# Optimization experiments

Hardware: AMD Instinct MI355X
Metric: run time of the kernel (lower is better)

Reference implementation:

```python
import jax, jax.numpy as jnp
import numpy as np

N, E = 100000, 400000
IN_DIM, PAD_DIM, HID = 384, 3, 64

def _xavier(key, fan_in, fan_out, shape=None):
    shape = shape or (fan_in, fan_out)
    lim = float(np.sqrt(6.0 / (fan_in + fan_out)))
    return jax.random.uniform(key, shape, jnp.float32, -lim, lim)

def setup_inputs():
    key = jax.random.key(0)
    ks = jax.random.split(key, 20)
    return {
        "x": jax.random.normal(ks[0], (N, IN_DIM), jnp.float32),
        "edge_index": jax.random.randint(ks[1], (2, E), 0, N),
        "pad_state": jax.random.uniform(ks[2], (PAD_DIM,), jnp.float32, -1.0, 1.0),
        # GAT layer 1: in = IN_DIM+PAD_DIM, heads=4, out=HID per head
        "W1": _xavier(ks[3], IN_DIM + PAD_DIM, 4 * HID),
        "att_src1": _xavier(ks[4], HID, HID, (4, HID)),
        "att_dst1": _xavier(ks[5], HID, HID, (4, HID)),
        "b1": jnp.zeros((4 * HID,), jnp.float32),
        # GAT layer 2: in = 4*HID, heads=2
        "W2": _xavier(ks[6], 4 * HID, 2 * HID),
        "att_src2": _xavier(ks[7], HID, HID, (2, HID)),
        "att_dst2": _xavier(ks[8], HID, HID, (2, HID)),
        "b2": jnp.zeros((2 * HID,), jnp.float32),
        # attention-score MLP
        "aw1": _xavier(ks[9], 2 * HID, HID),
        "ab1": jnp.zeros((HID,), jnp.float32),
        "aw2": _xavier(ks[10], HID, 1),
        "ab2": jnp.zeros((1,), jnp.float32),
        # emotion gate
        "gw": _xavier(ks[11], PAD_DIM, HID),
        "gb": jnp.zeros((HID,), jnp.float32),
    }

def _gat(h_in, src, dst, W, a_src, a_dst, bias, heads):
    # PyG GATConv (eval mode): linear -> per-head LeakyReLU attention logits
    # -> edge softmax over destination -> scatter-add aggregation -> concat heads + bias
    n = h_in.shape[0]
    h = (h_in @ W).reshape(n, heads, -1)               # [N,H,C]
    al_s = jnp.einsum('nhc,hc->nh', h, a_src)          # [N,H]
    al_d = jnp.einsum('nhc,hc->nh', h, a_dst)
    e = jax.nn.leaky_relu(al_s[src] + al_d[dst], 0.2)  # [Etot,H]
    m = jax.ops.segment_max(e, dst, num_segments=n)    # stable softmax per dst
    p = jnp.exp(e - m[dst])
    denom = jax.ops.segment_sum(p, dst, num_segments=n)
    coef = p / (denom[dst] + 1e-16)
    out = jax.ops.segment_sum(h[src] * coef[:, :, None], dst, num_segments=n)
    return out.reshape(n, -1) + bias

def reference(x, edge_index, pad_state, W1, att_src1, att_dst1, b1,
              W2, att_src2, att_dst2, b2, aw1, ab1, aw2, ab2, gw, gb):
    n = x.shape[0]
    loops = jnp.arange(n, dtype=edge_index.dtype)      # add_self_loops=True default
    src = jnp.concatenate([edge_index[0], loops])
    dst = jnp.concatenate([edge_index[1], loops])
    pad_exp = jnp.broadcast_to(pad_state.reshape(1, -1), (n, pad_state.size))
    h = jnp.concatenate([x, pad_exp], axis=-1)         # [N, in_dim+pad_dim]
    h = jax.nn.elu(_gat(h, src, dst, W1, att_src1, att_dst1, b1, 4))
    h = jax.nn.elu(_gat(h, src, dst, W2, att_src2, att_dst2, b2, 2))
    gate = jax.nn.sigmoid(pad_exp @ gw + gb)           # [N,HID]
    h = h * jnp.tile(gate, (1, 2))                     # [N,2*HID]
    attn = jax.nn.sigmoid(jax.nn.relu(h @ aw1 + ab1) @ aw2 + ab2)  # [N,1]
    return h, attn
```

## Files before the change

kernel.cpp:

```cpp
#include <hip/hip_runtime.h>
#include <hip/hip_bf16.h>
#include <stdint.h>

#define IN_DIM 384
#define HID 64
#define C1 256
#define C2 128

typedef unsigned int uint32;
typedef __bf16 bf16x8 __attribute__((ext_vector_type(8)));
typedef float f32x4 __attribute__((ext_vector_type(4)));

static __device__ __forceinline__ float bf2f(unsigned short u){
    return __uint_as_float(((uint32)u) << 16);
}
static __device__ __forceinline__ unsigned short f2bf(float x){
    uint32 u = __float_as_uint(x);
    return (unsigned short)((u + 0x7FFFu + ((u >> 16) & 1u)) >> 16);
}
static __device__ __forceinline__ uint32 pack2(float a, float b){
    return (uint32)f2bf(a) | ((uint32)f2bf(b) << 16);
}

__global__ void k_zero(int* deg, int* cur, int N){
    int i = blockIdx.x*256 + threadIdx.x;
    if (i < N){ deg[i] = 0; cur[i] = 0; }
}
__global__ void k_hist(const int* __restrict__ ei, int* deg, int E){
    int i = blockIdx.x*256 + threadIdx.x;
    if (i < E) atomicAdd(&deg[ei[E + i]], 1);
}
__global__ void k_scan1(const int* __restrict__ deg, int* rowptr, int* part, int N){
    __shared__ int s[256];
    int tid = threadIdx.x;
    int i = blockIdx.x*256 + tid;
    int v = (i < N) ? deg[i] : 0;
    s[tid] = v; __syncthreads();
    for (int off = 1; off < 256; off <<= 1){
        int t = (tid >= off) ? s[tid - off] : 0;
        __syncthreads();
        s[tid] += t;
        __syncthreads();
    }
    if (i < N) rowptr[i] = s[tid] - v;
    if (tid == 255) part[blockIdx.x] = s[tid];
}
__global__ void k_scan2(int* part, int nb){
    __shared__ int s[512];
    int tid = threadIdx.x;
    int v = (tid < nb) ? part[tid] : 0;
    s[tid] = v; __syncthreads();
    for (int off = 1; off < 512; off <<= 1){
        int t = (tid >= off) ? s[tid - off] : 0;
        __syncthreads();
        s[tid] += t;
        __syncthreads();
    }
    if (tid < nb) part[tid] = s[tid] - v;
}
__global__ void k_scan3(int* rowptr, const int* __restrict__ part, int N, int E){
    int i = blockIdx.x*256 + threadIdx.x;
    if (i < N) rowptr[i] += part[blockIdx.x];
    if (i == 0) rowptr[N] = E;
}
__global__ void k_scatter(const int* __restrict__ ei, const int* __restrict__ rowptr,
                          int* cur, int* colx, int* dstx, int E){
    int i = blockIdx.x*256 + threadIdx.x;
    if (i < E){
        int d = ei[E + i];
        int pos = atomicAdd(&cur[d], 1);
        int p = rowptr[d] + pos;
        colx[p] = ei[i];
        dstx[p] = d;
    }
}

__global__ __launch_bounds__(256) void k_cvtW(const float* __restrict__ W,
        unsigned short* __restrict__ Wf, int ncol, int ntiles, int nunits){
    int unit = blockIdx.x*4 + (threadIdx.x >> 6);
    if (unit >= nunits) return;
    int l = threadIdx.x & 63;
    int s = unit / ntiles, ct = unit % ntiles;
    int col = ct*16 + (l & 15);
    int g = l >> 4;
    unsigned short o[8];
    #pragma unroll
    for (int j = 0; j < 8; j++){
        int k = s*32 + g*8 + j;
        o[j] = f2bf(W[(size_t)k*ncol + col]);
    }
    ushort4* dst = (ushort4*)&Wf[((size_t)unit*64 + l)*8];
    dst[0] = make_ushort4(o[0], o[1], o[2], o[3]);
    dst[1] = make_ushort4(o[4], o[5], o[6], o[7]);
}

__global__ __launch_bounds__(256) void k_prep(const float* __restrict__ W1,
        const float* __restrict__ pad, const float* __restrict__ gw, const float* __restrict__ gb,
        float* __restrict__ c1v, float* __restrict__ gate){
    int tid = threadIdx.x;
    c1v[tid] = pad[0]*W1[(size_t)(IN_DIM+0)*C1 + tid]
             + pad[1]*W1[(size_t)(IN_DIM+1)*C1 + tid]
             + pad[2]*W1[(size_t)(IN_DIM+2)*C1 + tid];
    if (tid < HID){
        float g = pad[0]*gw[0*HID + tid] + pad[1]*gw[1*HID + tid] + pad[2]*gw[2*HID + tid] + gb[tid];
        gate[tid] = 1.f/(1.f + __expf(-g));
    }
}

__global__ __launch_bounds__(256) void k_gemm1_mfma(const float* __restrict__ x,
        const unsigned short* __restrict__ Wf, const float* __restrict__ c1v,
        const float* __restrict__ as1, const float* __restrict__ ad1,
        unsigned short* __restrict__ h1, float* __restrict__ als, float* __restrict__ ald, int N)
{
    __shared__ unsigned short Af[12*4*64*8];
    const int tid = threadIdx.x;
    const int l   = tid & 63;
    const int w   = tid >> 6;
    const int n0  = blockIdx.x * 64;

    const int srow = w*16 + (l & 15);
    const int kc   = l >> 4;
    int crow = n0 + srow; if (crow > N-1) crow = N-1;
    const float* xr = x + (size_t)crow*IN_DIM + kc*8;

    float4 a0[12], a1[12];
    #pragma unroll
    for (int j = 0; j < 12; j++){
        a0[j] = *(const float4*)(xr + j*32);
        a1[j] = *(const float4*)(xr + j*32 + 4);
    }
    #pragma unroll
    for (int j = 0; j < 12; j++){
        uint4 u;
        u.x = pack2(a0[j].x, a0[j].y); u.y = pack2(a0[j].z, a0[j].w);
        u.z = pack2(a1[j].x, a1[j].y); u.w = pack2(a1[j].z, a1[j].w);
        *(uint4*)&Af[((j*4 + w)*64 + l)*8] = u;
    }

    f32x4 acc[4][4];
    #pragma unroll
    for (int i = 0; i < 4; i++)
        #pragma unroll
        for (int rt = 0; rt < 4; rt++)
            acc[i][rt] = (f32x4){0.f, 0.f, 0.f, 0.f};

    uint4 wcur[4], wnxt[4];
    {
        const unsigned short* p = Wf + ((size_t)(w*4)*64 + l)*8;
        #pragma unroll
        for (int i = 0; i < 4; i++) wcur[i] = *(const uint4*)(p + (size_t)i*512);
    }
    __syncthreads();

    for (int ku = 0; ku < 12; ++ku){
        if (ku < 11){
            const unsigned short* p = Wf + ((size_t)((ku+1)*16 + w*4)*64 + l)*8;
            #pragma unroll
            for (int i = 0; i < 4; i++) wnxt[i] = *(const uint4*)(p + (size_t)i*512);
        }
        bf16x8 af[4];
        #pragma unroll
        for (int rt = 0; rt < 4; rt++)
            af[rt] = __builtin_bit_cast(bf16x8, *(const uint4*)&Af[((ku*4 + rt)*64 + l)*8]);
        #pragma unroll
        for (int i = 0; i < 4; i++){
            bf16x8 bw = __builtin_bit_cast(bf16x8, wcur[i]);
            #pragma unroll
            for (int rt = 0; rt < 4; rt++)
                acc[i][rt] = __builtin_amdgcn_mfma_f32_16x16x32_bf16(bw, af[rt], acc[i][rt], 0, 0, 0);
        }
        if (ku < 11){
            #pragma unroll
            for (int i = 0; i < 4; i++) wcur[i] = wnxt[i];
        }
    }

    const int g = l >> 4;
    float4 cvv[4], av[4], dv[4];
    #pragma unroll
    for (int i = 0; i < 4; i++){
        int cl = i*16 + g*4;
        cvv[i] = *(const float4*)&c1v[w*64 + cl];
        av[i]  = *(const float4*)&as1[w*64 + cl];
        dv[i]  = *(const float4*)&ad1[w*64 + cl];
    }
    #pragma unroll
    for (int rt = 0; rt < 4; rt++){
        int node = n0 + rt*16 + (l & 15);
        bool ok = node < N;
        float ps = 0.f, pd = 0.f;
        #pragma unroll
        for (int i = 0; i < 4; i++){
            float h0 = acc[i][rt][0] + cvv[i].x;
            float h1v = acc[i][rt][1] + cvv[i].y;
            float h2v = acc[i][rt][2] + cvv[i].z;
            float h3v = acc[i][rt][3] + cvv[i].w;
            ps += h0*av[i].x + h1v*av[i].y + h2v*av[i].z + h3v*av[i].w;
            pd += h0*dv[i].x + h1v*dv[i].y + h2v*dv[i].z + h3v*dv[i].w;
            if (ok){
                ushort4 o = make_ushort4(f2bf(h0), f2bf(h1v), f2bf(h2v), f2bf(h3v));
                *(ushort4*)&h1[(size_t)node*C1 + w*64 + i*16 + g*4] = o;
            }
        }
        ps += __shfl_xor(ps, 16, 64); ps += __shfl_xor(ps, 32, 64);
        pd += __shfl_xor(pd, 16, 64); pd += __shfl_xor(pd, 32, 64);
        if (ok && g == 0){
            als[(size_t)node*4 + w] = ps;
            ald[(size_t)node*4 + w] = pd;
        }
    }
}

__global__ __launch_bounds__(256) void k_gemm2_mfma(const unsigned short* __restrict__ x2,
        const unsigned short* __restrict__ Wf,
        const float* __restrict__ as2, const float* __restrict__ ad2,
        unsigned short* __restrict__ h2, float* __restrict__ als, float* __restrict__ ald, int N)
{
    __shared__ unsigned short Af[2][4*64*8];
    const int tid = threadIdx.x;
    const int l   = tid & 63;
    const int w   = tid >> 6;
    const int wr  = w >> 1, wc = w & 1;
    const int n0  = blockIdx.x * 64;

    const int sr  = tid >> 2;
    const int kc  = tid & 3;
    const int d0  = ((sr >> 4)*64 + kc*16 + (sr & 15))*8;
    int crow = n0 + sr; if (crow > N-1) crow = N-1;
    const unsigned short* xrow = x2 + (size_t)crow*C1 + kc*8;

    f32x4 acc[4][2];
    #pragma unroll
    for (int i = 0; i < 4; i++)
        #pragma unroll
        for (int rt = 0; rt < 2; rt++)
            acc[i][rt] = (f32x4){0.f, 0.f, 0.f, 0.f};

    uint4 p0, wcur[4], wnxt[4];
    p0 = *(const uint4*)(xrow);
    *(uint4*)&Af[0][d0] = p0;
    {
        const unsigned short* p = Wf + ((size_t)(wc*4)*64 + l)*8;
        #pragma unroll
        for (int i = 0; i < 4; i++) wcur[i] = *(const uint4*)(p + (size_t)i*512);
    }
    __syncthreads();

    for (int s = 0; s < 8; ++s){
        if (s < 7){
            p0 = *(const uint4*)(xrow + (s+1)*32);
            const unsigned short* p = Wf + ((size_t)((s+1)*8 + wc*4)*64 + l)*8;
            #pragma unroll
            for (int i = 0; i < 4; i++) wnxt[i] = *(const uint4*)(p + (size_t)i*512);
        }
        bf16x8 af[2];
        #pragma unroll
        for (int rt = 0; rt < 2; rt++)
            af[rt] = __builtin_bit_cast(bf16x8, *(const uint4*)&Af[s&1][((wr*2 + rt)*64 + l)*8]);
        #pragma unroll
        for (int i = 0; i < 4; i++){
            bf16x8 bw = __builtin_bit_cast(bf16x8, wcur[i]);
            #pragma unroll
            for (int rt = 0; rt < 2; rt++)
                acc[i][rt] = __builtin_amdgcn_mfma_f32_16x16x32_bf16(bw, af[rt], acc[i][rt], 0, 0, 0);
        }
        if (s < 7){
            *(uint4*)&Af[(s+1)&1][d0] = p0;
            __syncthreads();
            #pragma unroll
            for (int i = 0; i < 4; i++) wcur[i] = wnxt[i];
        }
    }

    const int g = l >> 4;
    float4 av[4], dv[4];
    #pragma unroll
    for (int i = 0; i < 4; i++){
        int cl = i*16 + g*4;
        av[i] = *(const float4*)&as2[wc*64 + cl];
        dv[i] = *(const float4*)&ad2[wc*64 + cl];
    }
    #pragma unroll
    for (int rt = 0; rt < 2; rt++){
        int node = n0 + wr*32 + rt*16 + (l & 15);
        bool ok = node < N;
        float ps = 0.f, pd = 0.f;
        #pragma unroll
        for (int i = 0; i < 4; i++){
            float h0 = acc[i][rt][0], h1v = acc[i][rt][1];
            float h2v = acc[i][rt][2], h3v = acc[i][rt][3];
            ps += h0*av[i].x + h1v*av[i].y + h2v*av[i].z + h3v*av[i].w;
            pd += h0*dv[i].x + h1v*dv[i].y + h2v*dv[i].z + h3v*dv[i].w;
            if (ok){
                ushort4 o = make_ushort4(f2bf(h0), f2bf(h1v), f2bf(h2v), f2bf(h3v));
                *(ushort4*)&h2[(size_t)node*C2 + wc*64 + i*16 + g*4] = o;
            }
        }
        ps += __shfl_xor(ps, 16, 64); ps += __shfl_xor(ps, 32, 64);
        pd += __shfl_xor(pd, 16, 64); pd += __shfl_xor(pd, 32, 64);
        if (ok && g == 0){
            als[(size_t)node*2 + wc] = ps;
            ald[(size_t)node*2 + wc] = pd;
        }
    }
}

template<int H>
__global__ __launch_bounds__(256) void k_elogit(const int* __restrict__ colx,
        const int* __restrict__ dstx, const float* __restrict__ als,
        const float* __restrict__ ald, float* __restrict__ ep, int E)
{
    int i = blockIdx.x*256 + threadIdx.x;
    if (i >= E) return;
    int s = colx[i], d = dstx[i];
    if constexpr (H == 4){
        float4 a = *(const float4*)&als[(size_t)s*4];
        float4 b = *(const float4*)&ald[(size_t)d*4];
        float4 e;
        e.x = a.x + b.x; e.x = fmaxf(e.x, 0.2f*e.x);
        e.y = a.y + b.y; e.y = fmaxf(e.y, 0.2f*e.y);
        e.z = a.z + b.z; e.z = fmaxf(e.z, 0.2f*e.z);
        e.w = a.w + b.w; e.w = fmaxf(e.w, 0.2f*e.w);
        *(float4*)&ep[(size_t)i*4] = e;
    } else {
        float2 a = *(const float2*)&als[(size_t)s*2];
        float2 b = *(const float2*)&ald[(size_t)d*2];
        float2 e;
        e.x = a.x + b.x; e.x = fmaxf(e.x, 0.2f*e.x);
        e.y = a.y + b.y; e.y = fmaxf(e.y, 0.2f*e.y);
        *(float2*)&ep[(size_t)i*2] = e;
    }
}

template<int H>
__global__ __launch_bounds__(256) void k_segsm(const int* __restrict__ rowptr,
        const float* __restrict__ als, const float* __restrict__ ald,
        float* __restrict__ ep, float* __restrict__ den, float* __restrict__ pSelf, int NH)
{
    int t = blockIdx.x*256 + threadIdx.x;
    if (t >= NH) return;
    int node = t / H;
    int head = t - node*H;
    int base = rowptr[node];
    int cnt  = rowptr[node+1] - base;
    float es = als[t] + ald[t];
    es = fmaxf(es, 0.2f*es);
    float m = es;
    for (int j = 0; j < cnt; j++)
        m = fmaxf(m, ep[(size_t)(base + j)*H + head]);
    float ps = __expf(es - m);
    float dn = ps;
    for (int j = 0; j < cnt; j++){
        size_t idx = (size_t)(base + j)*H + head;
        float p = __expf(ep[idx] - m);
        ep[idx] = p;
        dn += p;
    }
    den[t]   = dn;
    pSelf[t] = ps;
}

template<int H, int CPL, int LAYER>
__global__ __launch_bounds__(256) void k_gat(const unsigned short* __restrict__ hlin,
        const float* __restrict__ ep, const float* __restrict__ den, const float* __restrict__ pSelf,
        const int* __restrict__ rowptr, const int* __restrict__ colx,
        const float* __restrict__ bias, const float* __restrict__ gate,
        unsigned short* __restrict__ out_bf, float* __restrict__ out_f, int N)
{
    constexpr int C = H*64;
    constexpr uint32 RB = C*2;
    int lane = threadIdx.x & 63, wid = threadIdx.x >> 6;
    int n = blockIdx.x*4 + wid;
    if (n >= N) return;
    const int c0 = lane*CPL;
    const int head = c0 >> 6;
    const int base = rowptr[n];
    const int cnt  = rowptr[n+1] - base;
    const char* hbase = (const char*)hlin + (uint32)c0*2;

    float acc[CPL];
    {
        float psf = pSelf[(uint32)n*H + head];
        if constexpr (CPL == 4){
            ushort4 v = *(const ushort4*)(hbase + (size_t)(uint32)n*RB);
            acc[0] = psf*bf2f(v.x); acc[1] = psf*bf2f(v.y);
            acc[2] = psf*bf2f(v.z); acc[3] = psf*bf2f(v.w);
        } else {
            uint32 v = *(const uint32*)(hbase + (size_t)(uint32)n*RB);
            acc[0] = psf*bf2f((unsigned short)(v & 0xffff));
            acc[1] = psf*bf2f((unsigned short)(v >> 16));
        }
    }
    for (int i = 0; i < cnt; i += 4){
        int idx[4], sk[4];
        #pragma unroll
        for (int k = 0; k < 4; k++){
            int ii = i + k; if (ii > cnt-1) ii = cnt-1;
            idx[k] = base + ii;
        }
        #pragma unroll
        for (int k = 0; k < 4; k++) sk[k] = colx[idx[k]];
        float pk[4];
        #pragma unroll
        for (int k = 0; k < 4; k++){
            float pv = ep[(size_t)(uint32)idx[k]*H + head];
            pk[k] = (i + k < cnt) ? pv : 0.f;
        }
        if constexpr (CPL == 4){
            ushort4 h4[4];
            #pragma unroll
            for (int k = 0; k < 4; k++) h4[k] = *(const ushort4*)(hbase + (size_t)(uint32)sk[k]*RB);
            #pragma unroll
            for (int k = 0; k < 4; k++){
                acc[0] += pk[k]*bf2f(h4[k].x);
                acc[1] += pk[k]*bf2f(h4[k].y);
                acc[2] += pk[k]*bf2f(h4[k].z);
                acc[3] += pk[k]*bf2f(h4[k].w);
            }
        } else {
            uint32 h2v[4];
            #pragma unroll
            for (int k = 0; k < 4; k++) h2v[k] = *(const uint32*)(hbase + (size_t)(uint32)sk[k]*RB);
            #pragma unroll
            for (int k = 0; k < 4; k++){
                acc[0] += pk[k]*bf2f((unsigned short)(h2v[k] & 0xffff));
                acc[1] += pk[k]*bf2f((unsigned short)(h2v[k] >> 16));
            }
        }
    }

    float inv = 1.f/(den[(uint32)n*H + head] + 1e-16f);
    if constexpr (LAYER == 1){
        unsigned short o[CPL];
        #pragma unroll
        for (int j = 0; j < CPL; j++){
            float r = acc[j]*inv + bias[c0 + j];
            r = (r > 0.f) ? r : (__expf(r) - 1.f);
            o[j] = f2bf(r);
        }
        if constexpr (CPL == 4){
            ushort4 ov; ov.x = o[0]; ov.y = o[1]; ov.z = o[2]; ov.w = o[3];
            *(ushort4*)&out_bf[(size_t)n*C + c0] = ov;
        }
    } else {
        float o[CPL];
        #pragma unroll
        for (int j = 0; j < CPL; j++){
            float r = acc[j]*inv + bias[c0 + j];
            r = (r > 0.f) ? r : (__expf(r) - 1.f);
            o[j] = r*gate[(c0 + j) & 63];
        }
        if constexpr (CPL == 2){
            *(float2*)&out_f[(size_t)n*C + c0] = make_float2(o[0], o[1]);
        }
    }
}

__global__ __launch_bounds__(256) void k_attn_mfma(const float* __restrict__ outh,
        const unsigned short* __restrict__ Wfa, const float* __restrict__ ab1,
        const float* __restrict__ aw2, const float* __restrict__ ab2,
        float* __restrict__ attn, int N)
{
    __shared__ unsigned short Af[4*8*64*8];
    const int tid = threadIdx.x;
    const int l   = tid & 63;
    const int w   = tid >> 6;
    const int n0  = blockIdx.x * 128;

    const int r  = tid >> 1;
    const int kh = tid & 1;
    const int rt8 = r >> 4, rr = r & 15;
    int crow = n0 + r; if (crow > N-1) crow = N-1;
    const float* src = outh + (size_t)crow*C2 + kh*16;
    #pragma unroll
    for (int s = 0; s < 4; s++){
        float4 a = *(const float4*)(src + s*32 + 0);
        float4 b = *(const float4*)(src + s*32 + 4);
        float4 c = *(const float4*)(src + s*32 + 8);
        float4 d = *(const float4*)(src + s*32 + 12);
        uint4 u0, u1;
        u0.x = pack2(a.x, a.y); u0.y = pack2(a.z, a.w);
        u0.z = pack2(b.x, b.y); u0.w = pack2(b.z, b.w);
        u1.x = pack2(c.x, c.y); u1.y = pack2(c.z, c.w);
        u1.z = pack2(d.x, d.y); u1.w = pack2(d.z, d.w);
        int d0 = ((s*8 + rt8)*64 + (kh*2)*16 + rr)*8;
        *(uint4*)&Af[d0]       = u0;
        *(uint4*)&Af[d0 + 128] = u1;
    }
    __syncthreads();

    f32x4 acc[4][2];
    #pragma unroll
    for (int i = 0; i < 4; i++)
        #pragma unroll
        for (int rt = 0; rt < 2; rt++)
            acc[i][rt] = (f32x4){0.f, 0.f, 0.f, 0.f};

    #pragma unroll
    for (int s = 0; s < 4; s++){
        bf16x8 af[2];
        #pragma unroll
        for (int rt = 0; rt < 2; rt++)
            af[rt] = __builtin_bit_cast(bf16x8, *(const uint4*)&Af[((s*8 + w*2 + rt)*64 + l)*8]);
        #pragma unroll
        for (int i = 0; i < 4; i++){
            bf16x8 bw = __builtin_bit_cast(bf16x8, *(const uint4*)&Wfa[((size_t)(s*4 + i)*64 + l)*8]);
            #pragma unroll
            for (int rt = 0; rt < 2; rt++)
                acc[i][rt] = __builtin_amdgcn_mfma_f32_16x16x32_bf16(bw, af[rt], acc[i][rt], 0, 0, 0);
        }
    }

    const int g = l >> 4;
    float4 abv[4], awv[4];
    #pragma unroll
    for (int i = 0; i < 4; i++){
        abv[i] = *(const float4*)&ab1[i*16 + g*4];
        awv[i] = *(const float4*)&aw2[i*16 + g*4];
    }
    float b2v = ab2[0];
    #pragma unroll
    for (int rt = 0; rt < 2; rt++){
        int node = n0 + (w*2 + rt)*16 + (l & 15);
        float part = 0.f;
        #pragma unroll
        for (int i = 0; i < 4; i++){
            float v0 = fmaxf(acc[i][rt][0] + abv[i].x, 0.f);
            float v1 = fmaxf(acc[i][rt][1] + abv[i].y, 0.f);
            float v2 = fmaxf(acc[i][rt][2] + abv[i].z, 0.f);
            float v3 = fmaxf(acc[i][rt][3] + abv[i].w, 0.f);
            part += v0*awv[i].x + v1*awv[i].y + v2*awv[i].z + v3*awv[i].w;
        }
        part += __shfl_xor(part, 16, 64);
        part += __shfl_xor(part, 32, 64);
        if (g == 0 && node < N)
            attn[node] = 1.f/(1.f + __expf(-(part + b2v)));
    }
}

extern "C" void kernel_launch(void* const* d_in, const int* in_sizes, int n_in,
                              void* d_out, int out_size, void* d_ws, size_t ws_size,
                              hipStream_t stream)
{
    const float* x    = (const float*)d_in[0];
    const int*   ei   = (const int*)  d_in[1];
    const float* pad  = (const float*)d_in[2];
    const float* W1   = (const float*)d_in[3];
    const float* as1  = (const float*)d_in[4];
    const float* ad1  = (const float*)d_in[5];
    const float* b1   = (const float*)d_in[6];
    const float* W2   = (const float*)d_in[7];
    const float* as2  = (const float*)d_in[8];
    const float* ad2  = (const float*)d_in[9];
    const float* b2   = (const float*)d_in[10];
    const float* aw1  = (const float*)d_in[11];
    const float* ab1  = (const float*)d_in[12];
    const float* aw2  = (const float*)d_in[13];
    const float* ab2  = (const float*)d_in[14];
    const float* gw   = (const float*)d_in[15];
    const float* gb   = (const float*)d_in[16];

    const int N = in_sizes[0] / IN_DIM;
    const int E = in_sizes[1] / 2;

    float* outh    = (float*)d_out;
    float* outattn = outh + (size_t)N*C2;

    char* w = (char*)d_ws;
    auto alloc = [&](size_t bytes)->char*{
        char* p = w;
        w += (bytes + 255) & ~(size_t)255;
        return p;
    };
    unsigned short* h1  = (unsigned short*)alloc((size_t)N*C1*2);
    unsigned short* x2  = (unsigned short*)alloc((size_t)N*C1*2);
    unsigned short* h2  = (unsigned short*)alloc((size_t)N*C2*2);
    float* als1 = (float*)alloc((size_t)N*4*4);
    float* ald1 = (float*)alloc((size_t)N*4*4);
    float* als2 = (float*)alloc((size_t)N*2*4);
    float* ald2 = (float*)alloc((size_t)N*2*4);
    int* deg    = (int*)alloc((size_t)N*4);
    int* cur    = (int*)alloc((size_t)N*4);
    int* rowptr = (int*)alloc((size_t)(N+1)*4);
    int* colx   = (int*)alloc((size_t)E*4);
    int* dstx   = (int*)alloc((size_t)E*4);
    int* part   = (int*)alloc(512*4);
    unsigned short* Wf1 = (unsigned short*)alloc((size_t)12*16*64*8*2);
    unsigned short* Wf2 = (unsigned short*)alloc((size_t)8*8*64*8*2);
    unsigned short* Wfa = (unsigned short*)alloc((size_t)4*4*64*8*2);
    float* c1v  = (float*)alloc(C1*4);
    float* gate = (float*)alloc(HID*4);

    float* ep1    = (float*)h2;
    float* den1   = (float*)((char*)h2 + (size_t)E*16);
    float* pSelf1 = (float*)((char*)h2 + (size_t)E*16 + (size_t)N*16);
    float* ep2    = (float*)x2;
    float* den2   = (float*)((char*)x2 + (size_t)E*8);
    float* pSelf2 = (float*)((char*)x2 + (size_t)E*8 + (size_t)N*8);

    const int nbN = (N + 255)/256;
    const int nbE = (E + 255)/256;
    const int nbW = (N + 3)/4;
    const int nbG = (N + 63)/64;
    const int nbA = (N + 127)/128;

    k_cvtW <<<(192+3)/4, 256, 0, stream>>>(W1, Wf1, C1, 16, 192);
    k_cvtW <<<(64+3)/4,  256, 0, stream>>>(W2, Wf2, C2, 8, 64);
    k_cvtW <<<(16+3)/4,  256, 0, stream>>>(aw1, Wfa, HID, 4, 16);
    k_prep <<<1, 256, 0, stream>>>(W1, pad, gw, gb, c1v, gate);

    k_zero   <<<nbN, 256, 0, stream>>>(deg, cur, N);
    k_hist   <<<nbE, 256, 0, stream>>>(ei, deg, E);
    k_scan1  <<<nbN, 256, 0, stream>>>(deg, rowptr, part, N);
    k_scan2  <<<1, 512, 0, stream>>>(part, nbN);
    k_scan3  <<<nbN, 256, 0, stream>>>(rowptr, part, N, E);
    k_scatter<<<nbE, 256, 0, stream>>>(ei, rowptr, cur, colx, dstx, E);

    k_gemm1_mfma<<<nbG, 256, 0, stream>>>(x, Wf1, c1v, as1, ad1, h1, als1, ald1, N);
    k_elogit<4><<<nbE, 256, 0, stream>>>(colx, dstx, als1, ald1, ep1, E);
    k_segsm<4> <<<(N*4 + 255)/256, 256, 0, stream>>>(rowptr, als1, ald1, ep1, den1, pSelf1, N*4);
    k_gat<4,4,1><<<nbW, 256, 0, stream>>>(h1, ep1, den1, pSelf1, rowptr, colx, b1,
                                          nullptr, x2, nullptr, N);

    k_gemm2_mfma<<<nbG, 256, 0, stream>>>(x2, Wf2, as2, ad2, h2, als2, ald2, N);
    k_elogit<2><<<nbE, 256, 0, stream>>>(colx, dstx, als2, ald2, ep2, E);
    k_segsm<2> <<<(N*2 + 255)/256, 256, 0, stream>>>(rowptr, als2, ald2, ep2, den2, pSelf2, N*2);
    k_gat<2,2,2><<<nbW, 256, 0, stream>>>(h2, ep2, den2, pSelf2, rowptr, colx, b2,
                                          gate, nullptr, outh, N);

    k_attn_mfma<<<nbA, 256, 0, stream>>>(outh, Wfa, ab1, aw2, ab2, outattn, N);
}
```

Measured before the change: 289.2 us.

## Pre-convert x to bf16 fragment layout and widen GEMM1 to 512 threads

Adds a separate kernel that converts the fp32 input x into bf16 already arranged in the MFMA fragment layout, stored in the x2 scratch buffer. GEMM1 then loads pre-packed bf16 tiles with coalesced 16-byte loads and runs 8 waves per block, split 2 row-groups by 4 column-groups, instead of 4 waves. The aim is to shrink GEMM1's load and convert phase and raise occupancy and latency hiding. The cost is an extra full pass over x: it is read in fp32 and written back as bf16 before being read again. An unused 64KB pad buffer is also allocated in the workspace, which shifts later allocation offsets.

```diff
diff --git a/kernel.cpp b/kernel.cpp
--- a/kernel.cpp
+++ b/kernel.cpp
@@ -94,6 +94,29 @@
     dst[1] = make_ushort4(o[4], o[5], o[6], o[7]);
 }
 
+__global__ __launch_bounds__(256) void k_cvtX(const float* __restrict__ x,
+        unsigned short* __restrict__ xs, int N){
+    const int blk = blockIdx.x;
+    const int n0  = blk*64;
+    const int t   = threadIdx.x;
+    unsigned short* dst = xs + (size_t)blk*24576;
+    #pragma unroll
+    for (int j = 0; j < 12; j++){
+        int c = j*256 + t;
+        int lane = c & 63, rt = (c >> 6) & 3, ku = c >> 8;
+        int row = rt*16 + (lane & 15);
+        int k0  = ku*32 + (lane >> 4)*8;
+        int n = n0 + row; if (n > N-1) n = N-1;
+        const float* src = x + (size_t)n*IN_DIM + k0;
+        float4 a = *(const float4*)src;
+        float4 b = *(const float4*)(src + 4);
+        uint4 u;
+        u.x = pack2(a.x, a.y); u.y = pack2(a.z, a.w);
+        u.z = pack2(b.x, b.y); u.w = pack2(b.z, b.w);
+        *(uint4*)(dst + (size_t)c*8) = u;
+    }
+}
+
 __global__ __launch_bounds__(256) void k_prep(const float* __restrict__ W1,
         const float* __restrict__ pad, const float* __restrict__ gw, const float* __restrict__ gb,
         float* __restrict__ c1v, float* __restrict__ gate){
@@ -107,46 +130,36 @@
     }
 }
 
-__global__ __launch_bounds__(256) void k_gemm1_mfma(const float* __restrict__ x,
+__global__ __launch_bounds__(512) void k_gemm1_mfma(const unsigned short* __restrict__ xs,
         const unsigned short* __restrict__ Wf, const float* __restrict__ c1v,
         const float* __restrict__ as1, const float* __restrict__ ad1,
         unsigned short* __restrict__ h1, float* __restrict__ als, float* __restrict__ ald, int N)
 {
-    __shared__ unsigned short Af[12*4*64*8];
+    __shared__ unsigned short Af[3072*8];
     const int tid = threadIdx.x;
     const int l   = tid & 63;
     const int w   = tid >> 6;
+    const int wr  = w >> 2;
+    const int wc  = w & 3;
     const int n0  = blockIdx.x * 64;
 
-    const int srow = w*16 + (l & 15);
-    const int kc   = l >> 4;
-    int crow = n0 + srow; if (crow > N-1) crow = N-1;
-    const float* xr = x + (size_t)crow*IN_DIM + kc*8;
-
-    float4 a0[12], a1[12];
-    #pragma unroll
-    for (int j = 0; j < 12; j++){
-        a0[j] = *(const float4*)(xr + j*32);
-        a1[j] = *(const float4*)(xr + j*32 + 4);
-    }
-    #pragma unroll
-    for (int j = 0; j < 12; j++){
-        uint4 u;
-        u.x = pack2(a0[j].x, a0[j].y); u.y = pack2(a0[j].z, a0[j].w);
-        u.z = pack2(a1[j].x, a1[j].y); u.w = pack2(a1[j].z, a1[j].w);
-        *(uint4*)&Af[((j*4 + w)*64 + l)*8] = u;
-    }
-
-    f32x4 acc[4][4];
+    const unsigned short* src = xs + (size_t)blockIdx.x*24576;
+    uint4 st[6];
+    #pragma unroll
+    for (int j = 0; j < 6; j++) st[j] = *(const uint4*)(src + (size_t)(j*512 + tid)*8);
+    #pragma unroll
+    for (int j = 0; j < 6; j++) *(uint4*)&Af[(size_t)(j*512 + tid)*8] = st[j];
+
+    f32x4 acc[4][2];
     #pragma unroll
     for (int i = 0; i < 4; i++)
         #pragma unroll
-        for (int rt = 0; rt < 4; rt++)
+        for (int rt = 0; rt < 2; rt++)
             acc[i][rt] = (f32x4){0.f, 0.f, 0.f, 0.f};
 
     uint4 wcur[4], wnxt[4];
     {
-        const unsigned short* p = Wf + ((size_t)(w*4)*64 + l)*8;
+        const unsigned short* p = Wf + ((size_t)(wc*4)*64 + l)*8;
         #pragma unroll
         for (int i = 0; i < 4; i++) wcur[i] = *(const uint4*)(p + (size_t)i*512);
     }
@@ -154,19 +167,19 @@
 
     for (int ku = 0; ku < 12; ++ku){
         if (ku < 11){
-            const unsigned short* p = Wf + ((size_t)((ku+1)*16 + w*4)*64 + l)*8;
+            const unsigned short* p = Wf + ((size_t)((ku+1)*16 + wc*4)*64 + l)*8;
             #pragma unroll
             for (int i = 0; i < 4; i++) wnxt[i] = *(const uint4*)(p + (size_t)i*512);
         }
-        bf16x8 af[4];
-        #pragma unroll
-        for (int rt = 0; rt < 4; rt++)
-            af[rt] = __builtin_bit_cast(bf16x8, *(const uint4*)&Af[((ku*4 + rt)*64 + l)*8]);
+        bf16x8 af[2];
+        #pragma unroll
+        for (int rt = 0; rt < 2; rt++)
+            af[rt] = __builtin_bit_cast(bf16x8, *(const uint4*)&Af[((ku*4 + wr*2 + rt)*64 + l)*8]);
         #pragma unroll
         for (int i = 0; i < 4; i++){
             bf16x8 bw = __builtin_bit_cast(bf16x8, wcur[i]);
             #pragma unroll
-            for (int rt = 0; rt < 4; rt++)
+            for (int rt = 0; rt < 2; rt++)
                 acc[i][rt] = __builtin_amdgcn_mfma_f32_16x16x32_bf16(bw, af[rt], acc[i][rt], 0, 0, 0);
         }
         if (ku < 11){
@@ -180,13 +193,13 @@
     #pragma unroll
     for (int i = 0; i < 4; i++){
         int cl = i*16 + g*4;
-        cvv[i] = *(const float4*)&c1v[w*64 + cl];
-        av[i]  = *(const float4*)&as1[w*64 + cl];
-        dv[i]  = *(const float4*)&ad1[w*64 + cl];
-    }
-    #pragma unroll
-    for (int rt = 0; rt < 4; rt++){
-        int node = n0 + rt*16 + (l & 15);
+        cvv[i] = *(const float4*)&c1v[wc*64 + cl];
+        av[i]  = *(const float4*)&as1[wc*64 + cl];
+        dv[i]  = *(const float4*)&ad1[wc*64 + cl];
+    }
+    #pragma unroll
+    for (int rt = 0; rt < 2; rt++){
+        int node = n0 + (wr*2 + rt)*16 + (l & 15);
         bool ok = node < N;
         float ps = 0.f, pd = 0.f;
         #pragma unroll
@@ -199,14 +212,14 @@
             pd += h0*dv[i].x + h1v*dv[i].y + h2v*dv[i].z + h3v*dv[i].w;
             if (ok){
                 ushort4 o = make_ushort4(f2bf(h0), f2bf(h1v), f2bf(h2v), f2bf(h3v));
-                *(ushort4*)&h1[(size_t)node*C1 + w*64 + i*16 + g*4] = o;
+                *(ushort4*)&h1[(size_t)node*C1 + wc*64 + i*16 + g*4] = o;
             }
         }
         ps += __shfl_xor(ps, 16, 64); ps += __shfl_xor(ps, 32, 64);
         pd += __shfl_xor(pd, 16, 64); pd += __shfl_xor(pd, 32, 64);
         if (ok && g == 0){
-            als[(size_t)node*4 + w] = ps;
-            ald[(size_t)node*4 + w] = pd;
+            als[(size_t)node*4 + wc] = ps;
+            ald[(size_t)node*4 + wc] = pd;
         }
     }
 }
@@ -575,6 +588,7 @@
     unsigned short* h1  = (unsigned short*)alloc((size_t)N*C1*2);
     unsigned short* x2  = (unsigned short*)alloc((size_t)N*C1*2);
     unsigned short* h2  = (unsigned short*)alloc((size_t)N*C2*2);
+    char*           xpad= alloc(65536);
     float* als1 = (float*)alloc((size_t)N*4*4);
     float* ald1 = (float*)alloc((size_t)N*4*4);
     float* als2 = (float*)alloc((size_t)N*2*4);
@@ -590,7 +604,9 @@
     unsigned short* Wfa = (unsigned short*)alloc((size_t)4*4*64*8*2);
     float* c1v  = (float*)alloc(C1*4);
     float* gate = (float*)alloc(HID*4);
-
+    (void)xpad;
+
+    unsigned short* xs = x2;
     float* ep1    = (float*)h2;
     float* den1   = (float*)((char*)h2 + (size_t)E*16);
     float* pSelf1 = (float*)((char*)h2 + (size_t)E*16 + (size_t)N*16);
@@ -609,6 +625,8 @@
     k_cvtW <<<(16+3)/4,  256, 0, stream>>>(aw1, Wfa, HID, 4, 16);
     k_prep <<<1, 256, 0, stream>>>(W1, pad, gw, gb, c1v, gate);
 
+    k_cvtX <<<nbG, 256, 0, stream>>>(x, xs, N);
+
     k_zero   <<<nbN, 256, 0, stream>>>(deg, cur, N);
     k_hist   <<<nbE, 256, 0, stream>>>(ei, deg, E);
     k_scan1  <<<nbN, 256, 0, stream>>>(deg, rowptr, part, N);
@@ -616,7 +634,7 @@
     k_scan3  <<<nbN, 256, 0, stream>>>(rowptr, part, N, E);
     k_scatter<<<nbE, 256, 0, stream>>>(ei, rowptr, cur, colx, dstx, E);
 
-    k_gemm1_mfma<<<nbG, 256, 0, stream>>>(x, Wf1, c1v, as1, ad1, h1, als1, ald1, N);
+    k_gemm1_mfma<<<nbG, 512, 0, stream>>>(xs, Wf1, c1v, as1, ad1, h1, als1, ald1, N);
     k_elogit<4><<<nbE, 256, 0, stream>>>(colx, dstx, als1, ald1, ep1, E);
     k_segsm<4> <<<(N*4 + 255)/256, 256, 0, stream>>>(rowptr, als1, ald1, ep1, den1, pSelf1, N*4);
     k_gat<4,4,1><<<nbW, 256, 0, stream>>>(h1, ep1, den1, pSelf1, rowptr, colx, b1,
```

Result: slower. 311.4 us (+7.7%).

## Stream x into LDS via global_load_lds with swizzle, halve gemm1 row tile

Applied to the files above, without the earlier changes.

Rewrites the first GEMM's A-operand staging so fp32 rows of x are copied straight from global memory into swizzled shared memory with global_load_lds, skipping the register round-trip. The bf16 conversion moves into the inner K loop. The row tile per block drops from 64 to 32 so the fp32 tile fits in LDS, which doubles the block count and the number of weight-fragment reloads. The aim is better overlap and throughput for the memory-bound x read, at the cost of repeated packing work and more redundant weight traffic.

```diff
diff --git a/kernel.cpp b/kernel.cpp
--- a/kernel.cpp
+++ b/kernel.cpp
@@ -10,6 +10,8 @@
 typedef unsigned int uint32;
 typedef __bf16 bf16x8 __attribute__((ext_vector_type(8)));
 typedef float f32x4 __attribute__((ext_vector_type(4)));
+typedef const __attribute__((address_space(1))) void* gas_ptr;
+typedef __attribute__((address_space(3))) void* las_ptr;
 
 static __device__ __forceinline__ float bf2f(unsigned short u){
     return __uint_as_float(((uint32)u) << 16);
@@ -112,36 +114,32 @@
         const float* __restrict__ as1, const float* __restrict__ ad1,
         unsigned short* __restrict__ h1, float* __restrict__ als, float* __restrict__ ald, int N)
 {
-    __shared__ unsigned short Af[12*4*64*8];
+    __shared__ float Afs[32*IN_DIM];
     const int tid = threadIdx.x;
     const int l   = tid & 63;
     const int w   = tid >> 6;
-    const int n0  = blockIdx.x * 64;
-
-    const int srow = w*16 + (l & 15);
-    const int kc   = l >> 4;
-    int crow = n0 + srow; if (crow > N-1) crow = N-1;
-    const float* xr = x + (size_t)crow*IN_DIM + kc*8;
-
-    float4 a0[12], a1[12];
-    #pragma unroll
-    for (int j = 0; j < 12; j++){
-        a0[j] = *(const float4*)(xr + j*32);
-        a1[j] = *(const float4*)(xr + j*32 + 4);
-    }
-    #pragma unroll
-    for (int j = 0; j < 12; j++){
-        uint4 u;
-        u.x = pack2(a0[j].x, a0[j].y); u.y = pack2(a0[j].z, a0[j].w);
-        u.z = pack2(a1[j].x, a1[j].y); u.w = pack2(a1[j].z, a1[j].w);
-        *(uint4*)&Af[((j*4 + w)*64 + l)*8] = u;
-    }
-
-    f32x4 acc[4][4];
+    const int n0  = blockIdx.x * 32;
+
+    const char* xg = (const char*)(x + (size_t)n0*IN_DIM);
+    #pragma unroll
+    for (int it = 0; it < 12; ++it){
+        int chunk = it*256 + tid;
+        int row   = chunk/96;
+        uint32 b  = (uint32)chunk*16;
+        uint32 s  = ((uint32)(row & 3)) << 5;
+        const char* src;
+        if (n0 + row < N) src = xg + (b ^ s);
+        else              src = (const char*)x;
+        uint32 ldsbase = (uint32)(it*256 + (tid & 0xFFC0))*16;
+        __builtin_amdgcn_global_load_lds((gas_ptr)src,
+                                         (las_ptr)((char*)Afs + ldsbase), 16, 0, 0);
+    }
+
+    f32x4 acc[4][2];
     #pragma unroll
     for (int i = 0; i < 4; i++)
         #pragma unroll
-        for (int rt = 0; rt < 4; rt++)
+        for (int rt = 0; rt < 2; rt++)
             acc[i][rt] = (f32x4){0.f, 0.f, 0.f, 0.f};
 
     uint4 wcur[4], wnxt[4];
@@ -152,21 +150,37 @@
     }
     __syncthreads();
 
+    const uint32 row0 = (uint32)(l & 15);
+    const uint32 row1 = row0 + 16;
+    const uint32 ad0  = (row0*1536 + ((uint32)(l >> 4))*32) ^ ((row0 & 3) << 5);
+    const uint32 ad1b = (row1*1536 + ((uint32)(l >> 4))*32) ^ ((row1 & 3) << 5);
+
     for (int ku = 0; ku < 12; ++ku){
         if (ku < 11){
             const unsigned short* p = Wf + ((size_t)((ku+1)*16 + w*4)*64 + l)*8;
             #pragma unroll
             for (int i = 0; i < 4; i++) wnxt[i] = *(const uint4*)(p + (size_t)i*512);
         }
-        bf16x8 af[4];
-        #pragma unroll
-        for (int rt = 0; rt < 4; rt++)
-            af[rt] = __builtin_bit_cast(bf16x8, *(const uint4*)&Af[((ku*4 + rt)*64 + l)*8]);
+        bf16x8 af[2];
+        {
+            float4 fa = *(const float4*)((const char*)Afs + ad0 + ku*128);
+            float4 fb = *(const float4*)((const char*)Afs + ad0 + ku*128 + 16);
+            uint4 u; u.x = pack2(fa.x, fa.y); u.y = pack2(fa.z, fa.w);
+            u.z = pack2(fb.x, fb.y); u.w = pack2(fb.z, fb.w);
+            af[0] = __builtin_bit_cast(bf16x8, u);
+        }
+        {
+            float4 fa = *(const float4*)((const char*)Afs + ad1b + ku*128);
+            float4 fb = *(const float4*)((const char*)Afs + ad1b + ku*128 + 16);
+            uint4 u; u.x = pack2(fa.x, fa.y); u.y = pack2(fa.z, fa.w);
+            u.z = pack2(fb.x, fb.y); u.w = pack2(fb.z, fb.w);
+            af[1] = __builtin_bit_cast(bf16x8, u);
+        }
         #pragma unroll
         for (int i = 0; i < 4; i++){
             bf16x8 bw = __builtin_bit_cast(bf16x8, wcur[i]);
             #pragma unroll
-            for (int rt = 0; rt < 4; rt++)
+            for (int rt = 0; rt < 2; rt++)
                 acc[i][rt] = __builtin_amdgcn_mfma_f32_16x16x32_bf16(bw, af[rt], acc[i][rt], 0, 0, 0);
         }
         if (ku < 11){
@@ -185,7 +199,7 @@
         dv[i]  = *(const float4*)&ad1[w*64 + cl];
     }
     #pragma unroll
-    for (int rt = 0; rt < 4; rt++){
+    for (int rt = 0; rt < 2; rt++){
         int node = n0 + rt*16 + (l & 15);
         bool ok = node < N;
         float ps = 0.f, pd = 0.f;
@@ -601,7 +615,8 @@
     const int nbN = (N + 255)/256;
     const int nbE = (E + 255)/256;
     const int nbW = (N + 3)/4;
-    const int nbG = (N + 63)/64;
+    const int nbG1 = (N + 31)/32;
+    const int nbG2 = (N + 63)/64;
     const int nbA = (N + 127)/128;
 
     k_cvtW <<<(192+3)/4, 256, 0, stream>>>(W1, Wf1, C1, 16, 192);
@@ -616,13 +631,13 @@
     k_scan3  <<<nbN, 256, 0, stream>>>(rowptr, part, N, E);
     k_scatter<<<nbE, 256, 0, stream>>>(ei, rowptr, cur, colx, dstx, E);
 
-    k_gemm1_mfma<<<nbG, 256, 0, stream>>>(x, Wf1, c1v, as1, ad1, h1, als1, ald1, N);
+    k_gemm1_mfma<<<nbG1, 256, 0, stream>>>(x, Wf1, c1v, as1, ad1, h1, als1, ald1, N);
     k_elogit<4><<<nbE, 256, 0, stream>>>(colx, dstx, als1, ald1, ep1, E);
     k_segsm<4> <<<(N*4 + 255)/256, 256, 0, stream>>>(rowptr, als1, ald1, ep1, den1, pSelf1, N*4);
     k_gat<4,4,1><<<nbW, 256, 0, stream>>>(h1, ep1, den1, pSelf1, rowptr, colx, b1,
                                           nullptr, x2, nullptr, N);
 
-    k_gemm2_mfma<<<nbG, 256, 0, stream>>>(x2, Wf2, as2, ad2, h2, als2, ald2, N);
+    k_gemm2_mfma<<<nbG2, 256, 0, stream>>>(x2, Wf2, as2, ad2, h2, als2, ald2, N);
     k_elogit<2><<<nbE, 256, 0, stream>>>(colx, dstx, als2, ald2, ep2, E);
     k_segsm<2> <<<(N*2 + 255)/256, 256, 0, stream>>>(rowptr, als2, ald2, ep2, den2, pSelf2, N*2);
     k_gat<2,2,2><<<nbW, 256, 0, stream>>>(h2, ep2, den2, pSelf2, rowptr, colx, b2,
```

After: 287.3 us. About the same (-0.6%).
